# Kernel optimization log

Measured on AMD Instinct MI355X. Metric: run time of the kernel, lower is better.

## Reference

```python
import jax, jax.numpy as jnp
import numpy as np

K = 96  # num_scales (conv kernel width)
PAD = K // 2


def setup_inputs() -> dict:
    key = jax.random.key(0)
    kx, kh, kl = jax.random.split(key, 3)
    x = jax.random.normal(kx, (64, 128, 4096), dtype=jnp.float32)
    h_w = jax.random.normal(kh, (1, 1, K), dtype=jnp.float32) * 0.1
    l_w = jax.random.normal(kl, (1, 1, K), dtype=jnp.float32) * 0.1
    return {"x": x, "h_w": h_w, "l_w": l_w}


def reference(x, h_w, l_w):
    # Original loops over channels applying the SAME Conv1d(1,1,K) to each
    # channel slice; this is exactly a depthwise conv with a shared filter.
    # Fold channels into the batch dim and run one conv per filter.
    B, C, T = x.shape
    xr = x.reshape(B * C, 1, T)  # [B*C, 1, T]

    def conv(w):
        # torch Conv1d is cross-correlation; lax conv matches (no kernel flip)
        y = jax.lax.conv_general_dilated(
            xr, w, window_strides=(1,), padding=[(PAD, PAD)],
            dimension_numbers=("NCH", "OIH", "NCH"))
        return y.reshape(B, C, -1)  # [B, C, T+1] for even K

    l_outs = conv(l_w)
    h_outs = conv(h_w)
    return (l_outs, h_outs)
```

## Files before the change

### kernel.cpp

```cpp
#include <hip/hip_runtime.h>


#define KW    96
#define PADW  48
#define T_IN  4096
#define T_OUT 4097
#define ROWS  8192
#define BLOCK 256
#define NF4   1056
#define XSH   (NF4 * 4)
#define BNC   320

typedef __attribute__((ext_vector_type(8))) short short8;
typedef __attribute__((ext_vector_type(4))) float f32x4;

__device__ __forceinline__ unsigned short f2bf(float v) {
    unsigned u = __builtin_bit_cast(unsigned, v);
    u += 0x7FFFu + ((u >> 16) & 1u);
    return (unsigned short)(u >> 16);
}

__global__ __launch_bounds__(BLOCK) void lwt_init(
    const float* __restrict__ hw, const float* __restrict__ lw,
    unsigned short* __restrict__ ws)
{
    const int t = threadIdx.x;
    const int L = t >> 2, c = t & 3;
    const int n = L & 15, q = L >> 4;
    const int s = n & 7, f = n >> 3;
    const float* w = f ? hw : lw;
    unsigned short b[8];
    #pragma unroll
    for (int j = 0; j < 8; ++j) {
        const int k = 32 * c + 8 * q + j;
        const int kk = k - s;
        b[j] = (kk >= 0 && kk < KW) ? f2bf(w[kk]) : (unsigned short)0;
    }
    uint4 pk;
    pk.x = (unsigned)b[0] | ((unsigned)b[1] << 16);
    pk.y = (unsigned)b[2] | ((unsigned)b[3] << 16);
    pk.z = (unsigned)b[4] | ((unsigned)b[5] << 16);
    pk.w = (unsigned)b[6] | ((unsigned)b[7] << 16);
    ((uint4*)ws)[t] = pk;
}

__global__ __launch_bounds__(BLOCK, 4) void lwt_main(
    const float* __restrict__ x,
    const float* __restrict__ hw,
    const float* __restrict__ lw,
    const unsigned short* __restrict__ ws,
    float* __restrict__ out_l,
    float* __restrict__ out_h)
{
    __shared__ alignas(16) unsigned short xs[XSH];
    __shared__ float bounce[4][2][BNC];
    const int bid = blockIdx.x;
    const int tid = threadIdx.x;

    if (bid < ROWS) {
        const int lane = tid & 63;

        const short8* wsB = (const short8*)ws;
        short8 bf0 = wsB[lane * 4 + 0];
        short8 bf1 = wsB[lane * 4 + 1];
        short8 bf2 = wsB[lane * 4 + 2];
        short8 bf3 = wsB[lane * 4 + 3];

        const float* xrow = x + (size_t)bid * T_IN;
        for (int i = tid; i < NF4; i += BLOCK) {
            const int g = 4 * i - PADW;
            float4 v = make_float4(0.f, 0.f, 0.f, 0.f);
            if (g >= 0 && g < T_IN) v = *(const float4*)(xrow + g);
            ushort4 u;
            u.x = f2bf(v.x); u.y = f2bf(v.y); u.z = f2bf(v.z); u.w = f2bf(v.w);
            *(ushort4*)(xs + 4 * i) = u;
        }
        __syncthreads();

        const int wv = tid >> 6;
        const int m  = lane & 15;
        const int q  = lane >> 4;
        const int sD = m & 7;
        const int fD = m >> 3;
        const short8* ap = (const short8*)xs;
        float* bw = &bounce[wv][fD][0];
        const size_t ob = (size_t)bid * T_OUT + (size_t)wv * 1024;

        #pragma unroll 1
        for (int ph = 0; ph < 4; ++ph) {
            #pragma unroll
            for (int it = 0; it < 2; ++it) {
                const int tile = wv * 8 + ph * 2 + it;
                const int ga0 = tile * 16 + m + q;
                f32x4 acc = {0.f, 0.f, 0.f, 0.f};
                acc = __builtin_amdgcn_mfma_f32_16x16x32_bf16(ap[ga0     ], bf0, acc, 0, 0, 0);
                acc = __builtin_amdgcn_mfma_f32_16x16x32_bf16(ap[ga0 +  4], bf1, acc, 0, 0, 0);
                acc = __builtin_amdgcn_mfma_f32_16x16x32_bf16(ap[ga0 +  8], bf2, acc, 0, 0, 0);
                acc = __builtin_amdgcn_mfma_f32_16x16x32_bf16(ap[ga0 + 12], bf3, acc, 0, 0, 0);
                #pragma unroll
                for (int r = 0; r < 4; ++r) {
                    const int i0 = it * 128 + 32 * q + 8 * r + sD;
                    bw[i0 + 8 * (i0 >> 5)] = acc[r];
                }
            }
            const int tb = ph * 256;
            #pragma unroll
            for (int p = 0; p < 4; ++p) {
                const int i = lane + 64 * p;
                out_l[ob + tb + i] = bounce[wv][0][i + 8 * (i >> 5)];
            }
            #pragma unroll
            for (int p = 0; p < 4; ++p) {
                const int i = lane + 64 * p;
                out_h[ob + tb + i] = bounce[wv][1][i + 8 * (i >> 5)];
            }
        }
    } else {
        const int r = (bid - ROWS) * BLOCK + tid;
        if (r < ROWS) {
            const float* xp = x + (size_t)r * T_IN + (T_OUT - 1 - PADW);
            float al = 0.f, ah = 0.f;
            #pragma unroll
            for (int k = 0; k < PADW; ++k) {
                const float xv = xp[k];
                al = fmaf(xv, lw[k], al);
                ah = fmaf(xv, hw[k], ah);
            }
            const size_t o = (size_t)r * T_OUT + (T_OUT - 1);
            out_l[o] = al;
            out_h[o] = ah;
        }
    }
}

extern "C" void kernel_launch(void* const* d_in, const int* in_sizes, int n_in,
                              void* d_out, int out_size, void* d_ws, size_t ws_size,
                              hipStream_t stream) {
    const float* x  = (const float*)d_in[0];
    const float* hw = (const float*)d_in[1];
    const float* lw = (const float*)d_in[2];
    float* out_l = (float*)d_out;
    float* out_h = out_l + (size_t)ROWS * T_OUT;
    unsigned short* wsB = (unsigned short*)d_ws;

    lwt_init<<<1, BLOCK, 0, stream>>>(hw, lw, wsB);
    const int grid = ROWS + ROWS / BLOCK;
    lwt_main<<<grid, BLOCK, 0, stream>>>(x, hw, lw, wsB, out_l, out_h);
}
```

Baseline: 367.4 us.

## Align output stores to float4, build weights in-kernel, fold tail into main blocks

Output rows have odd length (4097), so row starts are not 16-byte aligned. The kernel now shifts each row's data in the shared bounce buffer by the row's alignment offset so each lane can issue aligned float4 global stores instead of scalar stores, with the unaligned head and tail elements written separately. The separate weight-packing kernel is removed and each block builds its bf16 B fragments from the weights directly. The extra tail blocks are dropped: the last output column is computed by one wave per row from the shared bf16 input with a shuffle reduction, which uses bf16-rounded inputs instead of fp32.

```diff
diff --git a/kernel.cpp b/kernel.cpp
--- a/kernel.cpp
+++ b/kernel.cpp
@@ -9,124 +9,129 @@
 #define BLOCK 256
 #define NF4   1056
 #define XSH   (NF4 * 4)
-#define BNC   320
+#define BSL   324
 
 typedef __attribute__((ext_vector_type(8))) short short8;
 typedef __attribute__((ext_vector_type(4))) float f32x4;
+typedef __attribute__((ext_vector_type(4))) unsigned int uint4v;
 
 __device__ __forceinline__ unsigned short f2bf(float v) {
     unsigned u = __builtin_bit_cast(unsigned, v);
     u += 0x7FFFu + ((u >> 16) & 1u);
     return (unsigned short)(u >> 16);
 }
-
-__global__ __launch_bounds__(BLOCK) void lwt_init(
-    const float* __restrict__ hw, const float* __restrict__ lw,
-    unsigned short* __restrict__ ws)
-{
-    const int t = threadIdx.x;
-    const int L = t >> 2, c = t & 3;
-    const int n = L & 15, q = L >> 4;
-    const int s = n & 7, f = n >> 3;
-    const float* w = f ? hw : lw;
-    unsigned short b[8];
-    #pragma unroll
-    for (int j = 0; j < 8; ++j) {
-        const int k = 32 * c + 8 * q + j;
-        const int kk = k - s;
-        b[j] = (kk >= 0 && kk < KW) ? f2bf(w[kk]) : (unsigned short)0;
-    }
-    uint4 pk;
-    pk.x = (unsigned)b[0] | ((unsigned)b[1] << 16);
-    pk.y = (unsigned)b[2] | ((unsigned)b[3] << 16);
-    pk.z = (unsigned)b[4] | ((unsigned)b[5] << 16);
-    pk.w = (unsigned)b[6] | ((unsigned)b[7] << 16);
-    ((uint4*)ws)[t] = pk;
+__device__ __forceinline__ float bf2f(unsigned short b) {
+    return __builtin_bit_cast(float, ((unsigned)b) << 16);
 }
 
 __global__ __launch_bounds__(BLOCK, 4) void lwt_main(
     const float* __restrict__ x,
     const float* __restrict__ hw,
     const float* __restrict__ lw,
-    const unsigned short* __restrict__ ws,
     float* __restrict__ out_l,
     float* __restrict__ out_h)
 {
     __shared__ alignas(16) unsigned short xs[XSH];
-    __shared__ float bounce[4][2][BNC];
-    const int bid = blockIdx.x;
-    const int tid = threadIdx.x;
+    __shared__ float bounce[4][2][BSL];
+    const int bid  = blockIdx.x;
+    const int tid  = threadIdx.x;
+    const int lane = tid & 63;
+    const int wv   = tid >> 6;
 
-    if (bid < ROWS) {
-        const int lane = tid & 63;
+    const int q  = lane >> 4;
+    const int nB = lane & 15;
+    const int sB = nB & 7;
+    const float* wf = (nB >> 3) ? hw : lw;
+    short8 bfr0, bfr1, bfr2, bfr3;
+#define BUILD_BF(dst, cc)                                                   \
+    {                                                                       \
+        uint4v u;                                                           \
+        _Pragma("unroll")                                                   \
+        for (int jj = 0; jj < 4; ++jj) {                                    \
+            const int k0 = 32 * (cc) + 8 * q + 2 * jj;                      \
+            const int ka = k0 - sB, kb = k0 + 1 - sB;                       \
+            const unsigned ba = (ka >= 0 && ka < KW) ? (unsigned)f2bf(wf[ka]) : 0u; \
+            const unsigned bb = (kb >= 0 && kb < KW) ? (unsigned)f2bf(wf[kb]) : 0u; \
+            u[jj] = ba | (bb << 16);                                        \
+        }                                                                   \
+        dst = __builtin_bit_cast(short8, u);                                \
+    }
+    BUILD_BF(bfr0, 0)
+    BUILD_BF(bfr1, 1)
+    BUILD_BF(bfr2, 2)
+    BUILD_BF(bfr3, 3)
+#undef BUILD_BF
 
-        const short8* wsB = (const short8*)ws;
-        short8 bf0 = wsB[lane * 4 + 0];
-        short8 bf1 = wsB[lane * 4 + 1];
-        short8 bf2 = wsB[lane * 4 + 2];
-        short8 bf3 = wsB[lane * 4 + 3];
+    const float* xrow = x + (size_t)bid * T_IN;
+    for (int i = tid; i < NF4; i += BLOCK) {
+        const int g = 4 * i - PADW;
+        float4 v = make_float4(0.f, 0.f, 0.f, 0.f);
+        if (g >= 0 && g < T_IN) v = *(const float4*)(xrow + g);
+        ushort4 u;
+        u.x = f2bf(v.x); u.y = f2bf(v.y); u.z = f2bf(v.z); u.w = f2bf(v.w);
+        *(ushort4*)(xs + 4 * i) = u;
+    }
+    __syncthreads();
 
-        const float* xrow = x + (size_t)bid * T_IN;
-        for (int i = tid; i < NF4; i += BLOCK) {
-            const int g = 4 * i - PADW;
-            float4 v = make_float4(0.f, 0.f, 0.f, 0.f);
-            if (g >= 0 && g < T_IN) v = *(const float4*)(xrow + g);
-            ushort4 u;
-            u.x = f2bf(v.x); u.y = f2bf(v.y); u.z = f2bf(v.z); u.w = f2bf(v.w);
-            *(ushort4*)(xs + 4 * i) = u;
-        }
-        __syncthreads();
+    const int m   = nB;
+    const int sD  = nB & 7;
+    const int fD  = nB >> 3;
+    const int cpos = bid & 3;
+    const size_t O = (size_t)bid * T_OUT + (size_t)wv * 1024;
+    const int phi4 = 4 * lane + 8 * ((4 * lane) >> 5);
+    const short8* ap = (const short8*)xs;
+    float* bw_s = &bounce[wv][fD][0];
+    float* opl  = out_l + O - cpos;
+    float* oph  = out_h + O - cpos;
 
-        const int wv = tid >> 6;
-        const int m  = lane & 15;
-        const int q  = lane >> 4;
-        const int sD = m & 7;
-        const int fD = m >> 3;
-        const short8* ap = (const short8*)xs;
-        float* bw = &bounce[wv][fD][0];
-        const size_t ob = (size_t)bid * T_OUT + (size_t)wv * 1024;
-
-        #pragma unroll 1
-        for (int ph = 0; ph < 4; ++ph) {
+    #pragma unroll 1
+    for (int ph = 0; ph < 4; ++ph) {
+        #pragma unroll
+        for (int it = 0; it < 2; ++it) {
+            const int tile = wv * 8 + ph * 2 + it;
+            const int ga0 = tile * 16 + m + q;
+            f32x4 acc = {0.f, 0.f, 0.f, 0.f};
+            acc = __builtin_amdgcn_mfma_f32_16x16x32_bf16(ap[ga0     ], bfr0, acc, 0, 0, 0);
+            acc = __builtin_amdgcn_mfma_f32_16x16x32_bf16(ap[ga0 +  4], bfr1, acc, 0, 0, 0);
+            acc = __builtin_amdgcn_mfma_f32_16x16x32_bf16(ap[ga0 +  8], bfr2, acc, 0, 0, 0);
+            acc = __builtin_amdgcn_mfma_f32_16x16x32_bf16(ap[ga0 + 12], bfr3, acc, 0, 0, 0);
             #pragma unroll
-            for (int it = 0; it < 2; ++it) {
-                const int tile = wv * 8 + ph * 2 + it;
-                const int ga0 = tile * 16 + m + q;
-                f32x4 acc = {0.f, 0.f, 0.f, 0.f};
-                acc = __builtin_amdgcn_mfma_f32_16x16x32_bf16(ap[ga0     ], bf0, acc, 0, 0, 0);
-                acc = __builtin_amdgcn_mfma_f32_16x16x32_bf16(ap[ga0 +  4], bf1, acc, 0, 0, 0);
-                acc = __builtin_amdgcn_mfma_f32_16x16x32_bf16(ap[ga0 +  8], bf2, acc, 0, 0, 0);
-                acc = __builtin_amdgcn_mfma_f32_16x16x32_bf16(ap[ga0 + 12], bf3, acc, 0, 0, 0);
-                #pragma unroll
-                for (int r = 0; r < 4; ++r) {
-                    const int i0 = it * 128 + 32 * q + 8 * r + sD;
-                    bw[i0 + 8 * (i0 >> 5)] = acc[r];
-                }
-            }
-            const int tb = ph * 256;
-            #pragma unroll
-            for (int p = 0; p < 4; ++p) {
-                const int i = lane + 64 * p;
-                out_l[ob + tb + i] = bounce[wv][0][i + 8 * (i >> 5)];
-            }
-            #pragma unroll
-            for (int p = 0; p < 4; ++p) {
-                const int i = lane + 64 * p;
-                out_h[ob + tb + i] = bounce[wv][1][i + 8 * (i >> 5)];
+            for (int r = 0; r < 4; ++r) {
+                const int i0 = it * 128 + 32 * q + 8 * r + sD;
+                const int j  = cpos + i0;
+                bw_s[j + 8 * (j >> 5)] = acc[r];
             }
         }
-    } else {
-        const int r = (bid - ROWS) * BLOCK + tid;
-        if (r < ROWS) {
-            const float* xp = x + (size_t)r * T_IN + (T_OUT - 1 - PADW);
-            float al = 0.f, ah = 0.f;
-            #pragma unroll
-            for (int k = 0; k < PADW; ++k) {
-                const float xv = xp[k];
-                al = fmaf(xv, lw[k], al);
-                ah = fmaf(xv, hw[k], ah);
+        const bool skip0 = (cpos != 0) && (ph == 0) && (lane == 0);
+        #pragma unroll
+        for (int f = 0; f < 2; ++f) {
+            float* bw = &bounce[wv][f][0];
+            float* op = f ? oph : opl;
+            const float4 v = *(const float4*)&bw[phi4];
+            if (!skip0) *(float4*)(op + 256 * ph + 4 * lane) = v;
+            if (cpos != 0) {
+                float* orow = (f ? out_h : out_l) + O;
+                if (ph == 0 && lane < 4 - cpos) orow[lane] = bw[cpos + lane];
+                if (ph == 3 && lane < cpos)     orow[1024 - cpos + lane] = bw[320 + lane];
+                if (ph < 3 && lane < cpos)      bw[lane] = bw[320 + lane];
             }
-            const size_t o = (size_t)r * T_OUT + (T_OUT - 1);
+        }
+    }
+
+    if (wv == 3) {
+        float al = 0.f, ah = 0.f;
+        if (lane < PADW) {
+            const float xv = bf2f(xs[T_IN + lane]);
+            al = xv * lw[lane];
+            ah = xv * hw[lane];
+        }
+        #pragma unroll
+        for (int off = 32; off > 0; off >>= 1) {
+            al += __shfl_down(al, off);
+            ah += __shfl_down(ah, off);
+        }
+        if (lane == 0) {
+            const size_t o = (size_t)bid * T_OUT + T_IN;
             out_l[o] = al;
             out_h[o] = ah;
         }
@@ -141,9 +146,6 @@
     const float* lw = (const float*)d_in[2];
     float* out_l = (float*)d_out;
     float* out_h = out_l + (size_t)ROWS * T_OUT;
-    unsigned short* wsB = (unsigned short*)d_ws;
 
-    lwt_init<<<1, BLOCK, 0, stream>>>(hw, lw, wsB);
-    const int grid = ROWS + ROWS / BLOCK;
-    lwt_main<<<grid, BLOCK, 0, stream>>>(x, hw, lw, wsB, out_l, out_h);
+    lwt_main<<<ROWS, BLOCK, 0, stream>>>(x, hw, lw, out_l, out_h);
 }
```

Result: no change. 371.8 us (+1.2%).
